# Performance work log

Measured on AMD Instinct MI355X. Metric: run time of the kernel, lower is better.

## Reference

```python
import jax, jax.numpy as jnp
import numpy as np

EPS = 1e-5

def _bn(x, g, b, m, v):
    # eval-mode batchnorm, NCHW, per-channel params
    inv = g / jnp.sqrt(v + EPS)
    return x * inv[None, :, None, None] + (b - m * inv)[None, :, None, None]

def setup_inputs() -> dict:
    key = jax.random.key(0)
    ks = jax.random.split(key, 16)
    C = 64
    x = jax.random.normal(ks[0], (8, C, 64, 64), dtype=jnp.float32)
    w1 = jax.random.normal(ks[1], (C, C, 1, 1), dtype=jnp.float32) * 0.1
    w2 = jax.random.normal(ks[2], (C, 1, 3, 3), dtype=jnp.float32) * 0.1
    w3 = jax.random.normal(ks[3], (C, C, 1, 1), dtype=jnp.float32) * 0.1
    def bn_params(k):
        k1, k2, k3, k4 = jax.random.split(k, 4)
        return (jax.random.uniform(k1, (C,)) + 0.5,
                jax.random.normal(k2, (C,)) * 0.1,
                jax.random.normal(k3, (C,)) * 0.1,
                jax.random.uniform(k4, (C,)) + 0.5)
    g1, b1, m1, v1 = bn_params(ks[4])
    g2, b2, m2, v2 = bn_params(ks[5])
    g3, b3, m3, v3 = bn_params(ks[6])
    return {"x": x, "w1": w1, "bn1_g": g1, "bn1_b": b1, "bn1_m": m1, "bn1_v": v1,
            "w2": w2, "bn2_g": g2, "bn2_b": b2, "bn2_m": m2, "bn2_v": v2,
            "w3": w3, "bn3_g": g3, "bn3_b": b3, "bn3_m": m3, "bn3_v": v3}

def reference(x, w1, bn1_g, bn1_b, bn1_m, bn1_v,
              w2, bn2_g, bn2_b, bn2_m, bn2_v,
              w3, bn3_g, bn3_b, bn3_m, bn3_v):
    B, c, h, w = x.shape
    N = h * w
    # conv1 (1x1) + BN + ReLU -> V
    v = jnp.einsum('bchw,oc->bohw', x, w1[:, :, 0, 0])
    v = jax.nn.relu(_bn(v, bn1_g, bn1_b, bn1_m, bn1_v))
    # attention over spatial positions: Q=K=x, single head, dim=c
    Q = x.reshape(B, c, N)          # bdn
    V = v.reshape(B, c, N)          # bdm
    scores = jnp.einsum('bdn,bdm->bnm', Q, Q) / (c ** 0.5)  # [B,N,N]
    prob = jax.nn.softmax(scores, axis=-1)
    out = jnp.einsum('bnm,bdm->bdn', prob, V).reshape(B, c, h, w)
    # depthwise conv + BN + ReLU
    out = jax.lax.conv_general_dilated(
        out, w2, window_strides=(1, 1), padding='SAME',
        dimension_numbers=('NCHW', 'OIHW', 'NCHW'), feature_group_count=c)
    out = jax.nn.relu(_bn(out, bn2_g, bn2_b, bn2_m, bn2_v))
    # pointwise conv + BN
    out = jnp.einsum('bchw,oc->bohw', out, w3[:, :, 0, 0])
    out = _bn(out, bn3_g, bn3_b, bn3_m, bn3_v)
    # residual (stride==1 and in_size==out_size)
    return out + x
```

## Files before the change

kernel.cpp:

```cpp
#include <hip/hip_runtime.h>
#include <stdint.h>

typedef __attribute__((ext_vector_type(8)))  short s16x8;
typedef __attribute__((ext_vector_type(16))) float f32x16;
typedef __attribute__((ext_vector_type(2)))  unsigned u32x2;

union CvtI4 { int4 i; s16x8 s; };
union CvtU4 { uint4 u; s16x8 s; };

__device__ __forceinline__ unsigned f2bf(float f) {
    union { float f; unsigned u; } v; v.f = f;
    return (v.u + 0x7fffu + ((v.u >> 16) & 1u)) >> 16;
}

__device__ __forceinline__ unsigned packbf(float lo, float hi) {
    union { float f; unsigned u; } a0, a1;
    a0.f = lo; a1.f = hi;
    return __builtin_amdgcn_perm(a1.u + 0x8000u, a0.u + 0x8000u, 0x07060302u);
}

__global__ __launch_bounds__(256) void k_prep(
    const float* __restrict__ x, const float* __restrict__ w1,
    const float* __restrict__ g1, const float* __restrict__ b1,
    const float* __restrict__ m1, const float* __restrict__ v1,
    unsigned short* __restrict__ xTf, unsigned short* __restrict__ vbff)
{
    __shared__ float X[64 * 65];
    const int b    = blockIdx.x >> 7;
    const int n0g  = (blockIdx.x >> 1) & 63;
    const int n0   = n0g << 6;
    const int half = blockIdx.x & 1;
    const int tid  = threadIdx.x;
    const float QS = 0.42466090014400953f;

    {
        const int r = tid >> 6, nn = tid & 63;
        const float* xb = x + (size_t)b * 262144 + n0 + nn;
#pragma unroll
        for (int cc = 0; cc < 16; ++cc) {
            int c = cc * 4 + r;
            X[c * 65 + nn] = xb[(size_t)c * 4096];
        }
    }
    __syncthreads();

    {
        const int n8 = tid >> 3, c8 = tid & 7;
        const int kk = c8 >> 1, hb = c8 & 1;
        const int st = (n0g << 1) + half;
        const int N  = (half << 5) + n8;
        unsigned u[4];
#pragma unroll
        for (int j = 0; j < 4; ++j) {
            unsigned lo = f2bf(X[(c8 * 8 + 2 * j) * 65 + N] * QS);
            unsigned hi = f2bf(X[(c8 * 8 + 2 * j + 1) * 65 + N] * QS);
            u[j] = lo | (hi << 16);
        }
        uint4 pk; pk.x = u[0]; pk.y = u[1]; pk.z = u[2]; pk.w = u[3];
        *(uint4*)(xTf + ((((size_t)((b << 7) + st) << 2) + kk) << 9)
                      + ((n8 + (hb << 5)) << 3)) = pk;
    }

    {
        const int n = tid & 63, og = tid >> 6;
        float rX[64];
#pragma unroll
        for (int c = 0; c < 64; ++c) rX[c] = X[c * 65 + n];
        const int cn = n >> 3, e = n & 7;
        const int sS = cn >> 2, kslS = (cn >> 1) & 1, hb = cn & 1;
        unsigned short* vb = vbff +
            ((((size_t)((b << 6) + n0g) << 3) + (sS << 2) + (kslS << 1) + half) << 9) + e;
#pragma unroll 2
        for (int oo = 0; oo < 8; ++oo) {
            int o = (half << 5) + og * 8 + oo;
            float inv = g1[o] * rsqrtf(v1[o] + 1e-5f);
            float sh  = b1[o] - m1[o] * inv;
            float acc = 0.f;
#pragma unroll
            for (int c = 0; c < 64; ++c) acc = fmaf(w1[o * 64 + c], rX[c], acc);
            int lane = (og * 8 + oo) + (hb << 5);
            vb[lane << 3] = (unsigned short)f2bf(fmaxf(fmaf(acc, inv, sh), 0.f));
        }
    }
}

__global__ __launch_bounds__(1024, 4) void k_attn(
    const unsigned short* __restrict__ xTf, const unsigned short* __restrict__ vbff,
    unsigned short* __restrict__ outO)
{
    __shared__ float scr[16384];
    __shared__ float rsL[16][32];
    __shared__ float dnm[128];

    const int b   = blockIdx.x & 7;
    const int qg2 = blockIdx.x >> 3;
    const int tid = threadIdx.x;
    const int w = tid >> 6, lane = tid & 63;
    const int l31 = lane & 31, half = lane >> 5;
    const int qbase = qg2 << 7;
    const int qd = w & 7, par = w >> 3;
    const int s  = qd & 1;
    const int t2 = qd >> 1;

    s16x8 Bq[4];
    {
        const unsigned short* qB = xTf +
            (((size_t)((b << 7) + (qg2 << 2) + t2)) << 11) + (lane << 3);
#pragma unroll
        for (int kk = 0; kk < 4; ++kk) {
            CvtI4 c; c.i = *(const int4*)(qB + (kk << 9));
            Bq[kk] = c.s;
        }
    }

    const unsigned short* akB = xTf  + (((size_t)((b << 9) + (s << 2))) << 9) + (lane << 3);
    const unsigned short* bvB = vbff + (((size_t)((b << 9) + (s << 2))) << 9) + (lane << 3);

    f32x16 O[2];
#pragma unroll
    for (int dl = 0; dl < 2; ++dl)
#pragma unroll
        for (int r = 0; r < 16; ++r) O[dl][r] = 0.f;
    float rs = 0.f;

    for (int it = 0; it < 32; ++it) {
        const size_t toff = ((size_t)((it << 1) + par)) << 12;

        int4 ar[4], br[4];
#pragma unroll
        for (int kk = 0; kk < 4; ++kk) ar[kk] = *(const int4*)(akB + (kk << 9) + toff);
#pragma unroll
        for (int j = 0; j < 4; ++j)    br[j]  = *(const int4*)(bvB + (j << 9) + toff);

        f32x16 S = {0.f,0.f,0.f,0.f,0.f,0.f,0.f,0.f,0.f,0.f,0.f,0.f,0.f,0.f,0.f,0.f};
        __builtin_amdgcn_s_setprio(1);
        {
            CvtI4 c0; c0.i = ar[0]; S = __builtin_amdgcn_mfma_f32_32x32x16_bf16(c0.s, Bq[0], S, 0, 0, 0);
            CvtI4 c1; c1.i = ar[1]; S = __builtin_amdgcn_mfma_f32_32x32x16_bf16(c1.s, Bq[1], S, 0, 0, 0);
            CvtI4 c2; c2.i = ar[2]; S = __builtin_amdgcn_mfma_f32_32x32x16_bf16(c2.s, Bq[2], S, 0, 0, 0);
            CvtI4 c3; c3.i = ar[3]; S = __builtin_amdgcn_mfma_f32_32x32x16_bf16(c3.s, Bq[3], S, 0, 0, 0);
        }
        __builtin_amdgcn_s_setprio(0);

        uint2 G[4];
#pragma unroll
        for (int q = 0; q < 4; ++q) {
            float p0 = __builtin_amdgcn_exp2f(S[4*q+0]);
            float p1 = __builtin_amdgcn_exp2f(S[4*q+1]);
            float p2 = __builtin_amdgcn_exp2f(S[4*q+2]);
            float p3 = __builtin_amdgcn_exp2f(S[4*q+3]);
            rs += (p0 + p1) + (p2 + p3);
            G[q].x = packbf(p0, p1);
            G[q].y = packbf(p2, p3);
        }

        __builtin_amdgcn_s_setprio(1);
#pragma unroll
        for (int ksl = 0; ksl < 2; ++ksl) {
            u32x2 r0 = __builtin_amdgcn_permlane32_swap(G[2*ksl].x, G[2*ksl+1].x, false, false);
            u32x2 r1 = __builtin_amdgcn_permlane32_swap(G[2*ksl].y, G[2*ksl+1].y, false, false);
            CvtU4 ac;
            ac.u.x = r0.x; ac.u.y = r1.x; ac.u.z = r0.y; ac.u.w = r1.y;
            const s16x8 Ap = ac.s;
            CvtI4 v0; v0.i = br[2*ksl + 0];
            CvtI4 v1; v1.i = br[2*ksl + 1];
            O[0] = __builtin_amdgcn_mfma_f32_32x32x16_bf16(Ap, v0.s, O[0], 0, 0, 0);
            O[1] = __builtin_amdgcn_mfma_f32_32x32x16_bf16(Ap, v1.s, O[1], 0, 0, 0);
        }
        __builtin_amdgcn_s_setprio(0);
    }

    float* scrK = scr;
    float* scrV = scr + 8192;

    rs += __shfl_xor(rs, 32);
    if (half == 0) rsL[w][l31] = rs;

    if (par == 1) {
        float* rg = (qd < 4) ? (scrK + (qd << 11)) : (scrV + ((qd - 4) << 11));
#pragma unroll
        for (int dl = 0; dl < 2; ++dl)
#pragma unroll
            for (int r = 0; r < 16; ++r)
                rg[(dl << 10) + (r << 6) + lane] = O[dl][r];
    }
    __syncthreads();

    if (tid < 128) {
        int tt = tid >> 5, n32 = tid & 31;
        dnm[tid] = (rsL[(tt << 1) + 0][n32] + rsL[(tt << 1) + 1][n32]) +
                   (rsL[(tt << 1) + 8][n32] + rsL[(tt << 1) + 9][n32]);
    }
    if (par == 0) {
        float* rg = (qd < 4) ? (scrK + (qd << 11)) : (scrV + ((qd - 4) << 11));
#pragma unroll
        for (int dl = 0; dl < 2; ++dl)
#pragma unroll
            for (int r = 0; r < 16; ++r)
                O[dl][r] += rg[(dl << 10) + (r << 6) + lane];
    }
    __syncthreads();

    if (par == 0 && s == 1) {
#pragma unroll
        for (int dl = 0; dl < 2; ++dl)
#pragma unroll
            for (int r = 0; r < 16; ++r)
                scrK[(t2 << 11) + (dl << 10) + (r << 6) + lane] = O[dl][r];
    }
    __syncthreads();

    if (par == 0 && s == 0) {
        const int nb = (b << 12) + qbase;
#pragma unroll
        for (int dl = 0; dl < 2; ++dl)
#pragma unroll
            for (int r = 0; r < 16; ++r) {
                int rowoff = (r & 3) + ((r >> 2) << 3) + (half << 2);
                int n = (t2 << 5) + rowoff;
                float o = O[dl][r] + scrK[(t2 << 11) + (dl << 10) + (r << 6) + lane];
                outO[((size_t)(nb + n) << 6) + (dl << 5) + l31] =
                    (unsigned short)f2bf(o * (1.f / dnm[n]));
            }
    }
}

__global__ __launch_bounds__(256) void k_post(
    const unsigned short* __restrict__ Obase,
    const float* __restrict__ x,
    const float* __restrict__ w2,
    const float* __restrict__ g2, const float* __restrict__ b2,
    const float* __restrict__ m2, const float* __restrict__ v2,
    const float* __restrict__ w3,
    const float* __restrict__ g3, const float* __restrict__ b3,
    const float* __restrict__ m3, const float* __restrict__ v3,
    float* __restrict__ out)
{
    __shared__ float W[3][34 * 66];
    __shared__ float T2[32 * 66];

    const int b  = blockIdx.x >> 7;
    const int h  = (blockIdx.x >> 1) & 63;
    const int wh = blockIdx.x & 1;
    const int wbase = wh << 5;
    const int tid = threadIdx.x;

#pragma unroll
    for (int r = 0; r < 3; ++r) {
        int hh = h + r - 1;
#pragma unroll
        for (int i = 0; i < 2; ++i) {
            int lin = (i << 8) + tid;
            if (lin < 272) {
                int wl = lin >> 3, cg = lin & 7;
                int wg = wbase + wl - 1;
                float* Wd = &W[r][wl * 66 + (cg << 3)];
                if (hh >= 0 && hh <= 63 && wg >= 0 && wg <= 63) {
                    size_t npos = (size_t)((b << 12) + (hh << 6) + wg);
                    uint4 v = *(const uint4*)(Obase + (npos << 6) + (cg << 3));
                    union { float f; unsigned u; } t;
                    t.u = v.x << 16;         Wd[0] = t.f;
                    t.u = v.x & 0xFFFF0000u; Wd[1] = t.f;
                    t.u = v.y << 16;         Wd[2] = t.f;
                    t.u = v.y & 0xFFFF0000u; Wd[3] = t.f;
                    t.u = v.z << 16;         Wd[4] = t.f;
                    t.u = v.z & 0xFFFF0000u; Wd[5] = t.f;
                    t.u = v.w << 16;         Wd[6] = t.f;
                    t.u = v.w & 0xFFFF0000u; Wd[7] = t.f;
                } else {
#pragma unroll
                    for (int j = 0; j < 8; ++j) Wd[j] = 0.f;
                }
            }
        }
    }
    __syncthreads();

    const int w32 = tid & 31, cq = tid >> 5;
    float t8[8];
#pragma unroll
    for (int i = 0; i < 8; ++i) t8[i] = 0.f;

#pragma unroll
    for (int ky = 0; ky < 3; ++ky) {
#pragma unroll
        for (int kx = 0; kx < 3; ++kx) {
            const int k = ky * 3 + kx;
            const float* Wr = &W[ky][(w32 + kx) * 66 + (cq << 3)];
#pragma unroll
            for (int i = 0; i < 2; ++i) {
                float4 a = *(const float4*)(Wr + (i << 2));
                int c = (cq << 3) + (i << 2);
                t8[i * 4 + 0] = fmaf(w2[(c + 0) * 9 + k], a.x, t8[i * 4 + 0]);
                t8[i * 4 + 1] = fmaf(w2[(c + 1) * 9 + k], a.y, t8[i * 4 + 1]);
                t8[i * 4 + 2] = fmaf(w2[(c + 2) * 9 + k], a.z, t8[i * 4 + 2]);
                t8[i * 4 + 3] = fmaf(w2[(c + 3) * 9 + k], a.w, t8[i * 4 + 3]);
            }
        }
    }
#pragma unroll
    for (int i = 0; i < 8; ++i) {
        int c = (cq << 3) + i;
        float inv = g2[c] * rsqrtf(v2[c] + 1e-5f);
        float sh  = b2[c] - m2[c] * inv;
        T2[w32 * 66 + c] = fmaxf(fmaf(t8[i], inv, sh), 0.f);
    }
    __syncthreads();

    float rT[64];
#pragma unroll
    for (int c4 = 0; c4 < 16; ++c4)
        *(float4*)&rT[c4 << 2] = *(const float4*)&T2[w32 * 66 + (c4 << 2)];

    const int hw = (h << 6) + wbase + w32;
#pragma unroll 2
    for (int oo = 0; oo < 8; ++oo) {
        int o = (cq << 3) + oo;
        float inv = g3[o] * rsqrtf(v3[o] + 1e-5f);
        float sh  = b3[o] - m3[o] * inv;
        float acc = 0.f;
#pragma unroll
        for (int c = 0; c < 64; ++c) acc = fmaf(w3[o * 64 + c], rT[c], acc);
        size_t idx = (((size_t)((b << 6) + o)) << 12) + hw;
        out[idx] = fmaf(acc, inv, sh) + x[idx];
    }
}

extern "C" void kernel_launch(void* const* d_in, const int* in_sizes, int n_in,
                              void* d_out, int out_size, void* d_ws, size_t ws_size,
                              hipStream_t stream)
{
    const float* x  = (const float*)d_in[0];
    const float* w1 = (const float*)d_in[1];
    const float* g1 = (const float*)d_in[2];
    const float* b1 = (const float*)d_in[3];
    const float* m1 = (const float*)d_in[4];
    const float* v1 = (const float*)d_in[5];
    const float* w2 = (const float*)d_in[6];
    const float* g2 = (const float*)d_in[7];
    const float* b2 = (const float*)d_in[8];
    const float* m2 = (const float*)d_in[9];
    const float* v2 = (const float*)d_in[10];
    const float* w3 = (const float*)d_in[11];
    const float* g3 = (const float*)d_in[12];
    const float* b3 = (const float*)d_in[13];
    const float* m3 = (const float*)d_in[14];
    const float* v3 = (const float*)d_in[15];
    float* out = (float*)d_out;

    unsigned short* xTf  = (unsigned short*)d_ws;
    unsigned short* vbff = xTf + (size_t)8 * 4096 * 64;
    unsigned short* Obase = (unsigned short*)((char*)d_ws + (8u << 20));

    k_prep<<<1024, 256, 0, stream>>>(x, w1, g1, b1, m1, v1, xTf, vbff);
    k_attn<<<256, 1024, 0, stream>>>(xTf, vbff, Obase);
    k_post<<<1024, 256, 0, stream>>>(Obase, x, w2, g2, b2, m2, v2,
                                     w3, g3, b3, m3, v3, out);
}
```

Before: 180.9 us.

## Split attention into 64-query blocks with four-way key partitioning

Each attention block now handles 64 queries instead of 128, and its 16 waves split the key range four ways instead of two. The grid doubles to 512 blocks so more workgroups are spread across the GPU's compute units. Partial outputs are combined in a two-stage reduction through shared memory, which adds a barrier. The cost is that each query tile's Q loads are repeated across more blocks and the partial sums take more reduction work.

```diff
diff --git a/kernel.cpp b/kernel.cpp
--- a/kernel.cpp
+++ b/kernel.cpp
@@ -84,28 +84,28 @@
     }
 }
 
-__global__ __launch_bounds__(1024, 4) void k_attn(
+__global__ __launch_bounds__(1024, 8) void k_attn(
     const unsigned short* __restrict__ xTf, const unsigned short* __restrict__ vbff,
     unsigned short* __restrict__ outO)
 {
     __shared__ float scr[16384];
     __shared__ float rsL[16][32];
-    __shared__ float dnm[128];
+    __shared__ float dnm[64];
 
     const int b   = blockIdx.x & 7;
-    const int qg2 = blockIdx.x >> 3;
+    const int qg  = blockIdx.x >> 3;
     const int tid = threadIdx.x;
     const int w = tid >> 6, lane = tid & 63;
     const int l31 = lane & 31, half = lane >> 5;
-    const int qbase = qg2 << 7;
-    const int qd = w & 7, par = w >> 3;
+    const int qbase = qg << 6;
+    const int qd = w & 3, par = w >> 2;
     const int s  = qd & 1;
     const int t2 = qd >> 1;
 
     s16x8 Bq[4];
     {
         const unsigned short* qB = xTf +
-            (((size_t)((b << 7) + (qg2 << 2) + t2)) << 11) + (lane << 3);
+            (((size_t)((b << 7) + (qg << 1) + t2)) << 11) + (lane << 3);
 #pragma unroll
         for (int kk = 0; kk < 4; ++kk) {
             CvtI4 c; c.i = *(const int4*)(qB + (kk << 9));
@@ -123,8 +123,8 @@
         for (int r = 0; r < 16; ++r) O[dl][r] = 0.f;
     float rs = 0.f;
 
-    for (int it = 0; it < 32; ++it) {
-        const size_t toff = ((size_t)((it << 1) + par)) << 12;
+    for (int it = 0; it < 16; ++it) {
+        const size_t toff = ((size_t)((it << 2) + par)) << 12;
 
         int4 ar[4], br[4];
 #pragma unroll
@@ -170,14 +170,11 @@
         __builtin_amdgcn_s_setprio(0);
     }
 
-    float* scrK = scr;
-    float* scrV = scr + 8192;
-
     rs += __shfl_xor(rs, 32);
     if (half == 0) rsL[w][l31] = rs;
 
-    if (par == 1) {
-        float* rg = (qd < 4) ? (scrK + (qd << 11)) : (scrV + ((qd - 4) << 11));
+    if (par >= 2) {
+        float* rg = scr + (((qd << 1) + (par & 1)) << 11);
 #pragma unroll
         for (int dl = 0; dl < 2; ++dl)
 #pragma unroll
@@ -186,13 +183,17 @@
     }
     __syncthreads();
 
-    if (tid < 128) {
-        int tt = tid >> 5, n32 = tid & 31;
-        dnm[tid] = (rsL[(tt << 1) + 0][n32] + rsL[(tt << 1) + 1][n32]) +
-                   (rsL[(tt << 1) + 8][n32] + rsL[(tt << 1) + 9][n32]);
-    }
-    if (par == 0) {
-        float* rg = (qd < 4) ? (scrK + (qd << 11)) : (scrV + ((qd - 4) << 11));
+    if (tid < 64) {
+        int t2v = tid >> 5, n32 = tid & 31;
+        float a = 0.f;
+#pragma unroll
+        for (int pp = 0; pp < 4; ++pp)
+            a += rsL[(pp << 2) + (t2v << 1) + 0][n32] +
+                 rsL[(pp << 2) + (t2v << 1) + 1][n32];
+        dnm[tid] = a;
+    }
+    if (par < 2) {
+        float* rg = scr + (((qd << 1) + par) << 11);
 #pragma unroll
         for (int dl = 0; dl < 2; ++dl)
 #pragma unroll
@@ -201,24 +202,44 @@
     }
     __syncthreads();
 
-    if (par == 0 && s == 1) {
+    if (par == 1) {
+        float* rg = scr + (qd << 11);
 #pragma unroll
         for (int dl = 0; dl < 2; ++dl)
 #pragma unroll
             for (int r = 0; r < 16; ++r)
-                scrK[(t2 << 11) + (dl << 10) + (r << 6) + lane] = O[dl][r];
+                rg[(dl << 10) + (r << 6) + lane] = O[dl][r];
+    }
+    __syncthreads();
+
+    if (par == 0) {
+        float* rg = scr + (qd << 11);
+#pragma unroll
+        for (int dl = 0; dl < 2; ++dl)
+#pragma unroll
+            for (int r = 0; r < 16; ++r)
+                O[dl][r] += rg[(dl << 10) + (r << 6) + lane];
+        if (s == 1) {
+            float* rg2 = scr + ((4 + t2) << 11);
+#pragma unroll
+            for (int dl = 0; dl < 2; ++dl)
+#pragma unroll
+                for (int r = 0; r < 16; ++r)
+                    rg2[(dl << 10) + (r << 6) + lane] = O[dl][r];
+        }
     }
     __syncthreads();
 
     if (par == 0 && s == 0) {
         const int nb = (b << 12) + qbase;
+        float* rg2 = scr + ((4 + t2) << 11);
 #pragma unroll
         for (int dl = 0; dl < 2; ++dl)
 #pragma unroll
             for (int r = 0; r < 16; ++r) {
                 int rowoff = (r & 3) + ((r >> 2) << 3) + (half << 2);
                 int n = (t2 << 5) + rowoff;
-                float o = O[dl][r] + scrK[(t2 << 11) + (dl << 10) + (r << 6) + lane];
+                float o = O[dl][r] + rg2[(dl << 10) + (r << 6) + lane];
                 outO[((size_t)(nb + n) << 6) + (dl << 5) + l31] =
                     (unsigned short)f2bf(o * (1.f / dnm[n]));
             }
@@ -353,7 +374,7 @@
     unsigned short* Obase = (unsigned short*)((char*)d_ws + (8u << 20));
 
     k_prep<<<1024, 256, 0, stream>>>(x, w1, g1, b1, m1, v1, xTf, vbff);
-    k_attn<<<256, 1024, 0, stream>>>(xTf, vbff, Obase);
+    k_attn<<<512, 1024, 0, stream>>>(xTf, vbff, Obase);
     k_post<<<1024, 256, 0, stream>>>(Obase, x, w2, g2, b2, m2, v2,
                                      w3, g3, b3, m3, v3, out);
 }
```

After: 501.4 us. +177.2%, slower.
